# Kernel optimization log

Measured on AMD Instinct MI355X. Metric: run time of the kernel, lower is better.

The kernel has to match this reference:

```python
import jax, jax.numpy as jnp
import numpy as np

N_NODES = 50000
N_EDGES = 800000
N_GRAPHS = 128
HEADS = 4
NEG_SLOPE = 0.2


def gat_layer(x, src, dst, W, a_src, a_dst, b, n_nodes):
    # x: [N, Fin]; W: [Fin, H*Fout]; a_src/a_dst: [H, Fout]; b: [H*Fout]
    H, Fo = a_src.shape
    h = (x @ W).reshape(n_nodes, H, Fo)                      # [N, H, Fo]
    s_src = jnp.einsum('nhf,hf->nh', h, a_src)               # [N, H]
    s_dst = jnp.einsum('nhf,hf->nh', h, a_dst)               # [N, H]
    e = jax.nn.leaky_relu(s_src[src] + s_dst[dst], NEG_SLOPE)  # [E, H]
    # segment softmax over destination nodes
    emax = jax.ops.segment_max(e, dst, num_segments=n_nodes)
    ex = jnp.exp(e - emax[dst])
    denom = jax.ops.segment_sum(ex, dst, num_segments=n_nodes)
    alpha = ex / (denom[dst] + 1e-16)                        # [E, H]
    msg = h[src] * alpha[:, :, None]                         # [E, H, Fo]
    out = jax.ops.segment_sum(msg, dst, num_segments=n_nodes)
    return out.reshape(n_nodes, H * Fo) + b


def setup_inputs() -> dict:
    key = jax.random.key(0)
    ks = jax.random.split(key, 16)
    x = jax.random.normal(ks[0], (N_NODES, 128), dtype=jnp.float32)
    edge_index = jax.random.randint(ks[1], (2, N_EDGES), 0, N_NODES, dtype=jnp.int64 if jax.config.jax_enable_x64 else jnp.int32)
    batch_index = jnp.sort(jax.random.randint(ks[2], (N_NODES,), 0, N_GRAPHS))
    s = 0.1
    # layer 0: in=128 -> H=4, Fo=32  => hidden 128
    W0 = jax.random.normal(ks[3], (128, HEADS * 32), jnp.float32) * s
    a_src0 = jax.random.normal(ks[4], (HEADS, 32), jnp.float32) * s
    a_dst0 = jax.random.normal(ks[5], (HEADS, 32), jnp.float32) * s
    b0 = jnp.zeros((HEADS * 32,), jnp.float32)
    # layer 1: in=128 -> H=4, Fo=64 => hidden 256
    W1 = jax.random.normal(ks[6], (128, HEADS * 64), jnp.float32) * s
    a_src1 = jax.random.normal(ks[7], (HEADS, 64), jnp.float32) * s
    a_dst1 = jax.random.normal(ks[8], (HEADS, 64), jnp.float32) * s
    b1 = jnp.zeros((HEADS * 64,), jnp.float32)
    # layer 2: in=256 -> H=4, Fo=64 => hidden 256
    W2 = jax.random.normal(ks[9], (256, HEADS * 64), jnp.float32) * s
    a_src2 = jax.random.normal(ks[10], (HEADS, 64), jnp.float32) * s
    a_dst2 = jax.random.normal(ks[11], (HEADS, 64), jnp.float32) * s
    b2 = jnp.zeros((HEADS * 64,), jnp.float32)
    # readout linear: 512 -> 10
    Wout = jax.random.normal(ks[12], (512, 10), jnp.float32) * s
    bout = jnp.zeros((10,), jnp.float32)
    return dict(x=x, edge_index=edge_index, batch_index=batch_index,
                W0=W0, a_src0=a_src0, a_dst0=a_dst0, b0=b0,
                W1=W1, a_src1=a_src1, a_dst1=a_dst1, b1=b1,
                W2=W2, a_src2=a_src2, a_dst2=a_dst2, b2=b2,
                Wout=Wout, bout=bout)


def reference(x, edge_index, batch_index,
              W0, a_src0, a_dst0, b0,
              W1, a_src1, a_dst1, b1,
              W2, a_src2, a_dst2, b2,
              Wout, bout):
    n = x.shape[0]
    loops = jnp.arange(n, dtype=edge_index.dtype)
    src = jnp.concatenate([edge_index[0], loops])  # PyG add_self_loops
    dst = jnp.concatenate([edge_index[1], loops])
    h = jax.nn.relu(gat_layer(x, src, dst, W0, a_src0, a_dst0, b0, n))
    h = jax.nn.relu(gat_layer(h, src, dst, W1, a_src1, a_dst1, b1, n))
    h = jax.nn.relu(gat_layer(h, src, dst, W2, a_src2, a_dst2, b2, n))
    # global mean / max pool per graph
    ssum = jax.ops.segment_sum(h, batch_index, num_segments=N_GRAPHS)
    cnt = jax.ops.segment_sum(jnp.ones((n, 1), h.dtype), batch_index, num_segments=N_GRAPHS)
    gmean = ssum / jnp.maximum(cnt, 1.0)
    gmax = jax.ops.segment_max(h, batch_index, num_segments=N_GRAPHS)
    pooled = jnp.concatenate([gmean, gmax], axis=1)  # [G, 512]
    return pooled @ Wout + bout
```

## Files before the change

kernel.cpp:

```cpp
#include <hip/hip_runtime.h>
#include <cfloat>

#define N_NODES 50000
#define N_EDGES 800000
#define E_TOT   850000
#define NG      128
#define NH      4
#define CHUNK   782

typedef float f4 __attribute__((ext_vector_type(4)));
typedef float v4f __attribute__((ext_vector_type(4)));
typedef _Float16 h8v __attribute__((ext_vector_type(8)));

__global__ void count_dst_k(const int* __restrict__ ei, int* __restrict__ cnt) {
    int e = blockIdx.x * blockDim.x + threadIdx.x;
    if (e >= E_TOT) return;
    int d = (e < N_EDGES) ? ei[N_EDGES + e] : (e - N_EDGES);
    atomicAdd(&cnt[d], 1);
}

__global__ void scan_sums_k(const int* __restrict__ cnt, int* __restrict__ bsum) {
    int b = blockIdx.x;
    int start = b * CHUNK, end2 = min(start + CHUNK, N_NODES);
    int lane = threadIdx.x & 63, wv = threadIdx.x >> 6;
    int s = 0;
    for (int i = start + threadIdx.x; i < end2; i += 256) s += cnt[i];
    #pragma unroll
    for (int off = 32; off; off >>= 1) s += __shfl_xor(s, off);
    __shared__ int ws[4];
    if (lane == 0) ws[wv] = s;
    __syncthreads();
    if (threadIdx.x == 0) bsum[b] = ws[0] + ws[1] + ws[2] + ws[3];
}

__global__ void scan_off_k(int* __restrict__ bsum, int* __restrict__ row_ptr) {
    int lane = threadIdx.x;
    int v = bsum[lane];
    int s = v;
    #pragma unroll
    for (int off = 1; off < 64; off <<= 1) {
        int t = __shfl_up(s, off);
        if (lane >= off) s += t;
    }
    bsum[lane] = s - v;
    if (lane == 63) row_ptr[N_NODES] = s;
}

__global__ void scan_write_k(const int* __restrict__ cnt, const int* __restrict__ bsum,
                             int* __restrict__ row_ptr, int* __restrict__ cursor) {
    int b = blockIdx.x;
    int start = b * CHUNK, end2 = min(start + CHUNK, N_NODES);
    __shared__ int wsum[4];
    __shared__ int carry_sh;
    int lane = threadIdx.x & 63, wv = threadIdx.x >> 6;
    if (threadIdx.x == 0) carry_sh = bsum[b];
    __syncthreads();
    for (int base = start; base < end2; base += 256) {
        int i = base + threadIdx.x;
        int v = (i < end2) ? cnt[i] : 0;
        int s = v;
        #pragma unroll
        for (int off = 1; off < 64; off <<= 1) {
            int t = __shfl_up(s, off);
            if (lane >= off) s += t;
        }
        if (lane == 63) wsum[wv] = s;
        __syncthreads();
        int woff = 0;
        #pragma unroll
        for (int k = 0; k < 4; ++k) if (k < wv) woff += wsum[k];
        int carry = carry_sh;
        if (i < end2) { int rp = carry + woff + s - v; row_ptr[i] = rp; cursor[i] = rp; }
        __syncthreads();
        if (threadIdx.x == 0) carry_sh = carry + wsum[0] + wsum[1] + wsum[2] + wsum[3];
        __syncthreads();
    }
}

__global__ void fill_k(const int* __restrict__ ei, int* __restrict__ cursor,
                       int* __restrict__ col) {
    int e = blockIdx.x * blockDim.x + threadIdx.x;
    if (e >= E_TOT) return;
    int s, d;
    if (e < N_EDGES) { s = ei[e]; d = ei[N_EDGES + e]; }
    else { s = e - N_EDGES; d = s; }
    int slot = atomicAdd(&cursor[d], 1);
    __builtin_nontemporal_store(s, &col[slot]);
}

template<int K, int NOUT>
__global__ void pack_w_k(const float* __restrict__ W, _Float16* __restrict__ Wp) {
    constexpr int total = (NOUT / 16) * (K / 32) * 64;
    int t = blockIdx.x * blockDim.x + threadIdx.x;
    if (t >= total) return;
    int lane = t & 63;
    int rest = t >> 6;
    int ks = rest % (K / 32);
    int n  = rest / (K / 32);
    int colW = n * 16 + (lane & 15);
    int krow = ks * 32 + (lane >> 4) * 8;
    h8v v;
    #pragma unroll
    for (int j = 0; j < 8; ++j) v[j] = (_Float16)W[(size_t)(krow + j) * NOUT + colW];
    *(h8v*)(Wp + (size_t)t * 8) = v;
}

template<int K, int NOUT>
__global__ void pack_a_k(const float* __restrict__ W, const float* __restrict__ asrc,
                         const float* __restrict__ adst, _Float16* __restrict__ Wp) {
    constexpr int KS = K / 32;
    constexpr int NT = NOUT / 16;
    constexpr int Fo = NOUT / NH;
    int t = blockIdx.x * blockDim.x + threadIdx.x;
    if (t >= KS * 64) return;
    int ks = t >> 6, lane = t & 63;
    int colL = lane & 15;
    int krow = ks * 32 + ((lane >> 4) & 3) * 8;
    h8v v = {};
    if (colL < 8) {
        int hd = colL & 3;
        const float* av = (colL < 4) ? asrc : adst;
        #pragma unroll
        for (int j = 0; j < 8; ++j) {
            float s = 0.f;
            const float* wr = W + (size_t)(krow + j) * NOUT + hd * Fo;
            for (int f = 0; f < Fo; ++f) s += wr[f] * av[hd * Fo + f];
            v[j] = (_Float16)s;
        }
    }
    *(h8v*)(Wp + (size_t)((NT * KS + ks) * 64 + lane) * 8) = v;
}

template<int K, int NOUT, typename XT>
__global__ __launch_bounds__(256) void gemm_k(const XT* __restrict__ x,
                                              const _Float16* __restrict__ Wp,
                                              _Float16* __restrict__ outh,
                                              float* __restrict__ ssrc,
                                              float* __restrict__ sdst) {
    constexpr int SLICE = NOUT / 8;
    constexpr int KS  = K / 32;
    constexpr int NT  = NOUT / 16;
    constexpr int LK  = K + 8;
    __shared__ __align__(16) _Float16 xs[64 * LK];
    int row0 = blockIdx.x * 64;
    for (int seg = threadIdx.x; seg < 64 * K / 8; seg += 256) {
        int r = seg / (K / 8);
        int c = (seg % (K / 8)) * 8;
        h8v v = {};
        if (row0 + r < N_NODES) {
            if constexpr (sizeof(XT) == 2) {
                v = *(const h8v*)((const _Float16*)x + (size_t)(row0 + r) * K + c);
            } else {
                const float* xp = (const float*)x + (size_t)(row0 + r) * K + c;
                float4 a = *(const float4*)xp;
                float4 b = *(const float4*)(xp + 4);
                v[0] = (_Float16)a.x; v[1] = (_Float16)a.y;
                v[2] = (_Float16)a.z; v[3] = (_Float16)a.w;
                v[4] = (_Float16)b.x; v[5] = (_Float16)b.y;
                v[6] = (_Float16)b.z; v[7] = (_Float16)b.w;
            }
        }
        *(h8v*)(xs + r * LK + c) = v;
    }
    __syncthreads();
    int wv = threadIdx.x >> 6, lane = threadIdx.x & 63;
    int quad = lane >> 4, colL = lane & 15;
    int r0 = row0 + wv * 16;
    h8v afr[KS];
    #pragma unroll
    for (int ks = 0; ks < KS; ++ks)
        afr[ks] = *(const h8v*)(xs + (wv * 16 + colL) * LK + ks * 32 + quad * 8);
    const h8v* bp = (const h8v*)Wp;
    #pragma unroll
    for (int t = 0; t <= NT; ++t) {
        v4f acc = {};
        #pragma unroll
        for (int ks = 0; ks < KS; ++ks) {
            h8v bfr = bp[(size_t)(t * KS + ks) * 64 + lane];
            acc = __builtin_amdgcn_mfma_f32_16x16x32_f16(afr[ks], bfr, acc, 0, 0, 0);
        }
        if (t < NT) {
            int n0 = t * 16;
            int col = n0 + colL;
            int sl = n0 / SLICE;
            int so = col % SLICE;
            _Float16* op = outh + (size_t)sl * N_NODES * SLICE + so;
            #pragma unroll
            for (int reg = 0; reg < 4; ++reg) {
                int row = r0 + quad * 4 + reg;
                if (row < N_NODES) op[(size_t)row * SLICE] = (_Float16)acc[reg];
            }
        } else if (colL < 8) {
            int hd = colL & 3;
            float* sp = (colL < 4) ? ssrc : sdst;
            #pragma unroll
            for (int reg = 0; reg < 4; ++reg) {
                int row = r0 + quad * 4 + reg;
                if (row < N_NODES) sp[row * NH + hd] = acc[reg];
            }
        }
    }
}

__global__ __launch_bounds__(256) void alpha2_k(const float* __restrict__ ssrc,
                                                const float* __restrict__ sdst,
                                                const int* __restrict__ row_ptr,
                                                const int* __restrict__ col,
                                                float* __restrict__ alpha) {
    int wv = threadIdx.x >> 6, lane = threadIdx.x & 63;
    int grp = lane >> 4, lg = lane & 15;
    int v = blockIdx.x * 16 + wv * 4 + grp;
    if (v >= N_NODES) return;
    int beg = row_ptr[v], cnt = row_ptr[v + 1] - beg;
    f4 sdv = *(const f4*)(sdst + v * NH);
    float* pl0 = alpha + beg;
    float* pl1 = alpha + (size_t)E_TOT + beg;
    float* pl2 = alpha + (size_t)2 * E_TOT + beg;
    float* pl3 = alpha + (size_t)3 * E_TOT + beg;

    if (cnt <= 64) {
        f4 er[4];
        f4 m = {-FLT_MAX, -FLT_MAX, -FLT_MAX, -FLT_MAX};
        #pragma unroll
        for (int i = 0; i < 4; ++i) {
            int j = lg + i * 16;
            if (j < cnt) {
                int u = col[beg + j];
                f4 e = *(const f4*)(ssrc + u * NH) + sdv;
                #pragma unroll
                for (int c = 0; c < 4; ++c) e[c] = (e[c] > 0.f) ? e[c] : 0.2f * e[c];
                er[i] = e;
                #pragma unroll
                for (int c = 0; c < 4; ++c) m[c] = fmaxf(m[c], e[c]);
            }
        }
        #pragma unroll
        for (int off = 1; off < 16; off <<= 1)
            #pragma unroll
            for (int c = 0; c < 4; ++c) m[c] = fmaxf(m[c], __shfl_xor(m[c], off));
        f4 den = {};
        #pragma unroll
        for (int i = 0; i < 4; ++i) {
            int j = lg + i * 16;
            if (j < cnt) {
                f4 w;
                #pragma unroll
                for (int c = 0; c < 4; ++c) w[c] = __expf(er[i][c] - m[c]);
                er[i] = w;
                den += w;
            }
        }
        #pragma unroll
        for (int off = 1; off < 16; off <<= 1)
            #pragma unroll
            for (int c = 0; c < 4; ++c) den[c] += __shfl_xor(den[c], off);
        f4 inv;
        #pragma unroll
        for (int c = 0; c < 4; ++c) inv[c] = 1.f / (den[c] + 1e-16f);
        #pragma unroll
        for (int i = 0; i < 4; ++i) {
            int j = lg + i * 16;
            if (j < cnt) {
                pl0[j] = er[i][0] * inv[0];
                pl1[j] = er[i][1] * inv[1];
                pl2[j] = er[i][2] * inv[2];
                pl3[j] = er[i][3] * inv[3];
            }
        }
    } else {
        f4 m = {-FLT_MAX, -FLT_MAX, -FLT_MAX, -FLT_MAX};
        for (int j = lg; j < cnt; j += 16) {
            int u = col[beg + j];
            f4 e = *(const f4*)(ssrc + u * NH) + sdv;
            #pragma unroll
            for (int c = 0; c < 4; ++c) {
                e[c] = (e[c] > 0.f) ? e[c] : 0.2f * e[c];
                m[c] = fmaxf(m[c], e[c]);
            }
        }
        #pragma unroll
        for (int off = 1; off < 16; off <<= 1)
            #pragma unroll
            for (int c = 0; c < 4; ++c) m[c] = fmaxf(m[c], __shfl_xor(m[c], off));
        f4 den = {};
        for (int j = lg; j < cnt; j += 16) {
            int u = col[beg + j];
            f4 e = *(const f4*)(ssrc + u * NH) + sdv;
            #pragma unroll
            for (int c = 0; c < 4; ++c) {
                e[c] = (e[c] > 0.f) ? e[c] : 0.2f * e[c];
                den[c] += __expf(e[c] - m[c]);
            }
        }
        #pragma unroll
        for (int off = 1; off < 16; off <<= 1)
            #pragma unroll
            for (int c = 0; c < 4; ++c) den[c] += __shfl_xor(den[c], off);
        f4 inv;
        #pragma unroll
        for (int c = 0; c < 4; ++c) inv[c] = 1.f / (den[c] + 1e-16f);
        for (int j = lg; j < cnt; j += 16) {
            int u = col[beg + j];
            f4 e = *(const f4*)(ssrc + u * NH) + sdv;
            #pragma unroll
            for (int c = 0; c < 4; ++c) e[c] = (e[c] > 0.f) ? e[c] : 0.2f * e[c];
            pl0[j] = __expf(e[0] - m[0]) * inv[0];
            pl1[j] = __expf(e[1] - m[1]) * inv[1];
            pl2[j] = __expf(e[2] - m[2]) * inv[2];
            pl3[j] = __expf(e[3] - m[3]) * inv[3];
        }
    }
}

template<int HFo, int SLICE, int LPN>
__global__ __launch_bounds__(256) void agg4_k(const _Float16* __restrict__ hh,
                                              const float* __restrict__ alpha,
                                              const int* __restrict__ row_ptr,
                                              const int* __restrict__ col,
                                              const float* __restrict__ bias,
                                              _Float16* __restrict__ outH) {
    constexpr int Fo   = HFo / NH;
    constexpr int NPW  = 64 / LPN;
    constexpr int NPB  = 4 * NPW;
    constexpr int CAPW = NPW * 32;
    __shared__ int2 prS[4][CAPW];
    int s = blockIdx.x & 7;
    int g = blockIdx.x >> 3;
    int wv = threadIdx.x >> 6, lane = threadIdx.x & 63;
    int sub = lane / LPN, lq = lane % LPN;
    int vFirst = g * NPB + wv * NPW;
    if (vFirst >= N_NODES) return;
    int vCount = min(NPW, N_NODES - vFirst);
    int hd = (s * SLICE) / Fo;
    const float* ap = alpha + (size_t)hd * E_TOT;
    int begW = row_ptr[vFirst];
    int endW = row_ptr[vFirst + vCount];
    int len = endW - begW;
    bool active = sub < vCount;
    int v = vFirst + sub;
    int beg = 0, cnt = 0;
    if (active) { beg = row_ptr[v]; cnt = row_ptr[v + 1] - beg; }
    const _Float16* base = hh + (size_t)s * N_NODES * SLICE;
    unsigned fo = (unsigned)(lq * 8);
    float acc[8] = {};

    if (len <= CAPW) {
        for (int t = lane; t < len; t += 64)
            prS[wv][t] = make_int2(col[begW + t], __float_as_int(ap[begW + t]));
        __builtin_amdgcn_wave_barrier();
        int off = beg - begW;
        int j = 0;
        for (; j + 8 <= cnt; j += 8) {
            int u[8]; float w[8]; h8v hv[8];
            #pragma unroll
            for (int i = 0; i < 8; ++i) {
                int2 q = prS[wv][off + j + i];
                u[i] = q.x; w[i] = __int_as_float(q.y);
            }
            #pragma unroll
            for (int i = 0; i < 8; ++i)
                hv[i] = *(const h8v*)(base + ((unsigned)(u[i] * SLICE) + fo));
            #pragma unroll
            for (int i = 0; i < 8; ++i)
                #pragma unroll
                for (int c = 0; c < 8; ++c) acc[c] += w[i] * (float)hv[i][c];
        }
        for (; j < cnt; ++j) {
            int2 q = prS[wv][off + j];
            float w = __int_as_float(q.y);
            h8v hv = *(const h8v*)(base + ((unsigned)(q.x * SLICE) + fo));
            #pragma unroll
            for (int c = 0; c < 8; ++c) acc[c] += w * (float)hv[c];
        }
    } else {
        const int*   cp = col + beg;
        const float* app = ap + beg;
        for (int j = 0; j < cnt; ++j) {
            int u = cp[j];
            float w = app[j];
            h8v hv = *(const h8v*)(base + ((unsigned)(u * SLICE) + fo));
            #pragma unroll
            for (int c = 0; c < 8; ++c) acc[c] += w * (float)hv[c];
        }
    }
    if (active) {
        int f0 = s * SLICE + lq * 8;
        h8v res;
        #pragma unroll
        for (int c = 0; c < 8; ++c) res[c] = (_Float16)fmaxf(acc[c] + bias[f0 + c], 0.f);
        *(h8v*)(outH + (size_t)v * HFo + f0) = res;
    }
}

__global__ void pool_k(const _Float16* __restrict__ h, const int* __restrict__ batch,
                       float* __restrict__ gsum, float* __restrict__ gmax) {
    int f = threadIdx.x;
    int n0 = blockIdx.x * 32;
    int nend = min(n0 + 32, N_NODES);
    int cur = -1;
    float sa = 0.f, ma = 0.f;
    for (int n = n0; n < nend; ++n) {
        int g = batch[n];
        float val = (float)h[(size_t)n * 256 + f];
        if (g != cur) {
            if (cur >= 0) {
                atomicAdd(&gsum[cur * 256 + f], sa);
                atomicMax((int*)&gmax[cur * 256 + f], __float_as_int(ma));
            }
            cur = g; sa = 0.f; ma = 0.f;
        }
        sa += val;
        ma = fmaxf(ma, val);
    }
    if (cur >= 0) {
        atomicAdd(&gsum[cur * 256 + f], sa);
        atomicMax((int*)&gmax[cur * 256 + f], __float_as_int(ma));
    }
}

__global__ void gcnt_k(const int* __restrict__ batch, int* __restrict__ gcnt) {
    int g = threadIdx.x;
    if (g >= NG) return;
    int lo = 0, hi = N_NODES;
    while (lo < hi) { int mid = (lo + hi) >> 1; if (batch[mid] < g) lo = mid + 1; else hi = mid; }
    int b0 = lo;
    lo = 0; hi = N_NODES;
    while (lo < hi) { int mid = (lo + hi) >> 1; if (batch[mid] < g + 1) lo = mid + 1; else hi = mid; }
    gcnt[g] = lo - b0;
}

__global__ void readout_k(const float* __restrict__ gsum, const float* __restrict__ gmax,
                          const int* __restrict__ gcnt, const float* __restrict__ Wout,
                          const float* __restrict__ bout, float* __restrict__ out) {
    int g = blockIdx.x, lane = threadIdx.x;
    float inv = 1.f / fmaxf((float)gcnt[g], 1.f);
    float acc[10];
    #pragma unroll
    for (int j = 0; j < 10; ++j) acc[j] = 0.f;
    for (int f = lane; f < 512; f += 64) {
        float p = (f < 256) ? gsum[g * 256 + f] * inv : gmax[g * 256 + (f - 256)];
        #pragma unroll
        for (int j = 0; j < 10; ++j) acc[j] += p * Wout[f * 10 + j];
    }
    #pragma unroll
    for (int j = 0; j < 10; ++j) {
        float a = acc[j];
        #pragma unroll
        for (int off = 32; off; off >>= 1) a += __shfl_xor(a, off);
        if (lane == 0) out[g * 10 + j] = a + bout[j];
    }
}

extern "C" void kernel_launch(void* const* d_in, const int* in_sizes, int n_in,
                              void* d_out, int out_size, void* d_ws, size_t ws_size,
                              hipStream_t stream) {
    const float* x    = (const float*)d_in[0];
    const int*   ei   = (const int*)d_in[1];
    const int*   batch= (const int*)d_in[2];
    const float* W0   = (const float*)d_in[3];
    const float* as0  = (const float*)d_in[4];
    const float* ad0  = (const float*)d_in[5];
    const float* b0   = (const float*)d_in[6];
    const float* W1   = (const float*)d_in[7];
    const float* as1  = (const float*)d_in[8];
    const float* ad1  = (const float*)d_in[9];
    const float* b1   = (const float*)d_in[10];
    const float* W2   = (const float*)d_in[11];
    const float* as2  = (const float*)d_in[12];
    const float* ad2  = (const float*)d_in[13];
    const float* b2   = (const float*)d_in[14];
    const float* Wout = (const float*)d_in[15];
    const float* bout = (const float*)d_in[16];
    float* out = (float*)d_out;

    char* ws = (char*)d_ws;
    size_t o = 0;
    auto take = [&](size_t bytes) { size_t r = o; o += (bytes + 255) & ~(size_t)255; return r; };
    size_t cnt_o  = take((size_t)N_NODES * 4);
    size_t gsum_o = take((size_t)NG * 256 * 4);
    size_t gmax_o = take((size_t)NG * 256 * 4);
    size_t gcnt_o = take((size_t)NG * 4);
    size_t zero_bytes = o;
    size_t rp_o   = take((size_t)(N_NODES + 1) * 4);
    size_t cur_o  = take((size_t)N_NODES * 4);
    size_t bsum_o = take((size_t)64 * 4);
    size_t col_o  = take((size_t)E_TOT * 4);
    size_t ssrc_o = take((size_t)N_NODES * NH * 4);
    size_t sdst_o = take((size_t)N_NODES * NH * 4);
    size_t alp_o  = take((size_t)NH * E_TOT * 4);
    size_t hh_o   = take((size_t)N_NODES * 256 * 2);
    size_t bufH_o = take((size_t)N_NODES * 256 * 2);
    size_t wp0_o  = take((size_t)(8 + 1) * 4 * 64 * 8 * 2);
    size_t wp1_o  = take((size_t)(16 + 1) * 4 * 64 * 8 * 2);
    size_t wp2_o  = take((size_t)(16 + 1) * 8 * 64 * 8 * 2);

    int*      cnt    = (int*)(ws + cnt_o);
    float*    gsum   = (float*)(ws + gsum_o);
    float*    gmax   = (float*)(ws + gmax_o);
    int*      gcnt   = (int*)(ws + gcnt_o);
    int*      row_ptr= (int*)(ws + rp_o);
    int*      cursor = (int*)(ws + cur_o);
    int*      bsum   = (int*)(ws + bsum_o);
    int*      col    = (int*)(ws + col_o);
    float*    ssrc   = (float*)(ws + ssrc_o);
    float*    sdst   = (float*)(ws + sdst_o);
    float*    alpha  = (float*)(ws + alp_o);
    _Float16* hH     = (_Float16*)(ws + hh_o);
    _Float16* bufH   = (_Float16*)(ws + bufH_o);
    _Float16* Wp0    = (_Float16*)(ws + wp0_o);
    _Float16* Wp1    = (_Float16*)(ws + wp1_o);
    _Float16* Wp2    = (_Float16*)(ws + wp2_o);

    (void)hipMemsetAsync(ws, 0, zero_bytes, stream);

    count_dst_k<<<(E_TOT + 255) / 256, 256, 0, stream>>>(ei, cnt);
    scan_sums_k<<<64, 256, 0, stream>>>(cnt, bsum);
    scan_off_k<<<1, 64, 0, stream>>>(bsum, row_ptr);
    scan_write_k<<<64, 256, 0, stream>>>(cnt, bsum, row_ptr, cursor);
    fill_k<<<(E_TOT + 255) / 256, 256, 0, stream>>>(ei, cursor, col);

    pack_w_k<128, 128><<<8, 256, 0, stream>>>(W0, Wp0);
    pack_w_k<128, 256><<<16, 256, 0, stream>>>(W1, Wp1);
    pack_w_k<256, 256><<<32, 256, 0, stream>>>(W2, Wp2);
    pack_a_k<128, 128><<<1, 256, 0, stream>>>(W0, as0, ad0, Wp0);
    pack_a_k<128, 256><<<1, 256, 0, stream>>>(W1, as1, ad1, Wp1);
    pack_a_k<256, 256><<<2, 256, 0, stream>>>(W2, as2, ad2, Wp2);

    int gemm_grid  = (N_NODES + 63) / 64;
    int alpha_grid = (N_NODES + 15) / 16;
    int agg128_grid = 8 * ((N_NODES + 127) / 128);
    int agg256_grid = 8 * ((N_NODES + 63) / 64);

    gemm_k<128, 128, float><<<gemm_grid, 256, 0, stream>>>(x, Wp0, hH, ssrc, sdst);
    alpha2_k<<<alpha_grid, 256, 0, stream>>>(ssrc, sdst, row_ptr, col, alpha);
    agg4_k<128, 16, 2><<<agg128_grid, 256, 0, stream>>>(hH, alpha, row_ptr, col, b0, bufH);

    gemm_k<128, 256, _Float16><<<gemm_grid, 256, 0, stream>>>(bufH, Wp1, hH, ssrc, sdst);
    alpha2_k<<<alpha_grid, 256, 0, stream>>>(ssrc, sdst, row_ptr, col, alpha);
    agg4_k<256, 32, 4><<<agg256_grid, 256, 0, stream>>>(hH, alpha, row_ptr, col, b1, bufH);

    gemm_k<256, 256, _Float16><<<gemm_grid, 256, 0, stream>>>(bufH, Wp2, hH, ssrc, sdst);
    alpha2_k<<<alpha_grid, 256, 0, stream>>>(ssrc, sdst, row_ptr, col, alpha);
    agg4_k<256, 32, 4><<<agg256_grid, 256, 0, stream>>>(hH, alpha, row_ptr, col, b2, bufH);

    pool_k<<<(N_NODES + 31) / 32, 256, 0, stream>>>(bufH, batch, gsum, gmax);
    gcnt_k<<<1, 128, 0, stream>>>(batch, gcnt);
    readout_k<<<NG, 64, 0, stream>>>(gsum, gmax, gcnt, Wout, bout, out);
}
```

Measured before the change: 517.2 us.

## Merge pack and count launches, add direct-load fp16 GEMM, vectorize pooling

Merges the six weight-packing launches into two kernels and folds the per-graph node count into the readout kernel, which cuts the number of small launches. Adds a GEMM variant for the fp16 hidden layers that loads A fragments straight from global memory with no LDS staging and computes 128 rows per block, reusing each B fragment for two row tiles. Pooling now handles two features per thread with half2 loads and runs with 128 threads per block. The col store in fill_k drops its nontemporal hint. The costs are more registers in the new GEMM and uncoalesced global fragment loads in place of LDS reads.

Result: faster. 476.9 us (-7.8%).

```diff
diff --git a/kernel.cpp b/kernel.cpp
--- a/kernel.cpp
+++ b/kernel.cpp
@@ -10,6 +10,7 @@
 
 typedef float f4 __attribute__((ext_vector_type(4)));
 typedef float v4f __attribute__((ext_vector_type(4)));
+typedef _Float16 h2v __attribute__((ext_vector_type(2)));
 typedef _Float16 h8v __attribute__((ext_vector_type(8)));
 
 __global__ void count_dst_k(const int* __restrict__ ei, int* __restrict__ cnt) {
@@ -85,14 +86,13 @@
     if (e < N_EDGES) { s = ei[e]; d = ei[N_EDGES + e]; }
     else { s = e - N_EDGES; d = s; }
     int slot = atomicAdd(&cursor[d], 1);
-    __builtin_nontemporal_store(s, &col[slot]);
+    col[slot] = s;
 }
 
 template<int K, int NOUT>
-__global__ void pack_w_k(const float* __restrict__ W, _Float16* __restrict__ Wp) {
-    constexpr int total = (NOUT / 16) * (K / 32) * 64;
-    int t = blockIdx.x * blockDim.x + threadIdx.x;
-    if (t >= total) return;
+__device__ void pack_w_dev(const float* __restrict__ W, _Float16* __restrict__ Wp, int blk) {
+    int t = blk * 256 + threadIdx.x;
+    if (t >= (NOUT / 16) * (K / 32) * 64) return;
     int lane = t & 63;
     int rest = t >> 6;
     int ks = rest % (K / 32);
@@ -105,13 +105,22 @@
     *(h8v*)(Wp + (size_t)t * 8) = v;
 }
 
+__global__ void pack_w_all_k(const float* __restrict__ W0, const float* __restrict__ W1,
+                             const float* __restrict__ W2, _Float16* __restrict__ Wp0,
+                             _Float16* __restrict__ Wp1, _Float16* __restrict__ Wp2) {
+    int b = blockIdx.x;
+    if (b < 8)       pack_w_dev<128, 128>(W0, Wp0, b);
+    else if (b < 24) pack_w_dev<128, 256>(W1, Wp1, b - 8);
+    else             pack_w_dev<256, 256>(W2, Wp2, b - 24);
+}
+
 template<int K, int NOUT>
-__global__ void pack_a_k(const float* __restrict__ W, const float* __restrict__ asrc,
-                         const float* __restrict__ adst, _Float16* __restrict__ Wp) {
+__device__ void pack_a_dev(const float* __restrict__ W, const float* __restrict__ asrc,
+                           const float* __restrict__ adst, _Float16* __restrict__ Wp, int blk) {
     constexpr int KS = K / 32;
     constexpr int NT = NOUT / 16;
     constexpr int Fo = NOUT / NH;
-    int t = blockIdx.x * blockDim.x + threadIdx.x;
+    int t = blk * 256 + threadIdx.x;
     if (t >= KS * 64) return;
     int ks = t >> 6, lane = t & 63;
     int colL = lane & 15;
@@ -131,8 +140,20 @@
     *(h8v*)(Wp + (size_t)((NT * KS + ks) * 64 + lane) * 8) = v;
 }
 
-template<int K, int NOUT, typename XT>
-__global__ __launch_bounds__(256) void gemm_k(const XT* __restrict__ x,
+__global__ void pack_a_all_k(const float* __restrict__ W0, const float* __restrict__ as0,
+                             const float* __restrict__ ad0, _Float16* __restrict__ Wp0,
+                             const float* __restrict__ W1, const float* __restrict__ as1,
+                             const float* __restrict__ ad1, _Float16* __restrict__ Wp1,
+                             const float* __restrict__ W2, const float* __restrict__ as2,
+                             const float* __restrict__ ad2, _Float16* __restrict__ Wp2) {
+    int b = blockIdx.x;
+    if (b == 0)      pack_a_dev<128, 128>(W0, as0, ad0, Wp0, 0);
+    else if (b == 1) pack_a_dev<128, 256>(W1, as1, ad1, Wp1, 0);
+    else             pack_a_dev<256, 256>(W2, as2, ad2, Wp2, b - 2);
+}
+
+template<int K, int NOUT>
+__global__ __launch_bounds__(256) void gemm_k(const float* __restrict__ x,
                                               const _Float16* __restrict__ Wp,
                                               _Float16* __restrict__ outh,
                                               float* __restrict__ ssrc,
@@ -148,17 +169,13 @@
         int c = (seg % (K / 8)) * 8;
         h8v v = {};
         if (row0 + r < N_NODES) {
-            if constexpr (sizeof(XT) == 2) {
-                v = *(const h8v*)((const _Float16*)x + (size_t)(row0 + r) * K + c);
-            } else {
-                const float* xp = (const float*)x + (size_t)(row0 + r) * K + c;
-                float4 a = *(const float4*)xp;
-                float4 b = *(const float4*)(xp + 4);
-                v[0] = (_Float16)a.x; v[1] = (_Float16)a.y;
-                v[2] = (_Float16)a.z; v[3] = (_Float16)a.w;
-                v[4] = (_Float16)b.x; v[5] = (_Float16)b.y;
-                v[6] = (_Float16)b.z; v[7] = (_Float16)b.w;
-            }
+            const float* xp = x + (size_t)(row0 + r) * K + c;
+            float4 a = *(const float4*)xp;
+            float4 b = *(const float4*)(xp + 4);
+            v[0] = (_Float16)a.x; v[1] = (_Float16)a.y;
+            v[2] = (_Float16)a.z; v[3] = (_Float16)a.w;
+            v[4] = (_Float16)b.x; v[5] = (_Float16)b.y;
+            v[6] = (_Float16)b.z; v[7] = (_Float16)b.w;
         }
         *(h8v*)(xs + r * LK + c) = v;
     }
@@ -197,6 +214,65 @@
             for (int reg = 0; reg < 4; ++reg) {
                 int row = r0 + quad * 4 + reg;
                 if (row < N_NODES) sp[row * NH + hd] = acc[reg];
+            }
+        }
+    }
+}
+
+template<int K, int NOUT>
+__global__ __launch_bounds__(256) void gemm_h_k(const _Float16* __restrict__ x,
+                                                const _Float16* __restrict__ Wp,
+                                                _Float16* __restrict__ outh,
+                                                float* __restrict__ ssrc,
+                                                float* __restrict__ sdst) {
+    constexpr int SLICE = NOUT / 8;
+    constexpr int KS = K / 32;
+    constexpr int NT = NOUT / 16;
+    int wv = threadIdx.x >> 6, lane = threadIdx.x & 63;
+    int quad = lane >> 4, colL = lane & 15;
+    int row0 = blockIdx.x * 128;
+    int r0a = row0 + wv * 16;
+    int r0b = row0 + 64 + wv * 16;
+    int rA = min(r0a + colL, N_NODES - 1);
+    int rB = min(r0b + colL, N_NODES - 1);
+    h8v afrA[KS], afrB[KS];
+    #pragma unroll
+    for (int ks = 0; ks < KS; ++ks) {
+        afrA[ks] = *(const h8v*)(x + (size_t)rA * K + ks * 32 + quad * 8);
+        afrB[ks] = *(const h8v*)(x + (size_t)rB * K + ks * 32 + quad * 8);
+    }
+    const h8v* bp = (const h8v*)Wp;
+    #pragma unroll
+    for (int t = 0; t <= NT; ++t) {
+        v4f accA = {}, accB = {};
+        #pragma unroll
+        for (int ks = 0; ks < KS; ++ks) {
+            h8v bfr = bp[(size_t)(t * KS + ks) * 64 + lane];
+            accA = __builtin_amdgcn_mfma_f32_16x16x32_f16(afrA[ks], bfr, accA, 0, 0, 0);
+            accB = __builtin_amdgcn_mfma_f32_16x16x32_f16(afrB[ks], bfr, accB, 0, 0, 0);
+        }
+        if (t < NT) {
+            int n0 = t * 16;
+            int col = n0 + colL;
+            int sl = n0 / SLICE;
+            int so = col % SLICE;
+            _Float16* op = outh + (size_t)sl * N_NODES * SLICE + so;
+            #pragma unroll
+            for (int reg = 0; reg < 4; ++reg) {
+                int rowA = r0a + quad * 4 + reg;
+                int rowB = r0b + quad * 4 + reg;
+                if (rowA < N_NODES) op[(size_t)rowA * SLICE] = (_Float16)accA[reg];
+                if (rowB < N_NODES) op[(size_t)rowB * SLICE] = (_Float16)accB[reg];
+            }
+        } else if (colL < 8) {
+            int hd = colL & 3;
+            float* sp = (colL < 4) ? ssrc : sdst;
+            #pragma unroll
+            for (int reg = 0; reg < 4; ++reg) {
+                int rowA = r0a + quad * 4 + reg;
+                int rowB = r0b + quad * 4 + reg;
+                if (rowA < N_NODES) sp[rowA * NH + hd] = accA[reg];
+                if (rowB < N_NODES) sp[rowB * NH + hd] = accB[reg];
             }
         }
     }
@@ -394,46 +470,45 @@
 
 __global__ void pool_k(const _Float16* __restrict__ h, const int* __restrict__ batch,
                        float* __restrict__ gsum, float* __restrict__ gmax) {
-    int f = threadIdx.x;
+    int f2 = threadIdx.x * 2;
     int n0 = blockIdx.x * 32;
     int nend = min(n0 + 32, N_NODES);
     int cur = -1;
-    float sa = 0.f, ma = 0.f;
+    float sa0 = 0.f, sa1 = 0.f, ma0 = 0.f, ma1 = 0.f;
     for (int n = n0; n < nend; ++n) {
         int g = batch[n];
-        float val = (float)h[(size_t)n * 256 + f];
+        h2v val = *(const h2v*)(h + (size_t)n * 256 + f2);
+        float v0 = (float)val[0], v1 = (float)val[1];
         if (g != cur) {
             if (cur >= 0) {
-                atomicAdd(&gsum[cur * 256 + f], sa);
-                atomicMax((int*)&gmax[cur * 256 + f], __float_as_int(ma));
-            }
-            cur = g; sa = 0.f; ma = 0.f;
-        }
-        sa += val;
-        ma = fmaxf(ma, val);
+                atomicAdd(&gsum[cur * 256 + f2], sa0);
+                atomicAdd(&gsum[cur * 256 + f2 + 1], sa1);
+                atomicMax((int*)&gmax[cur * 256 + f2], __float_as_int(ma0));
+                atomicMax((int*)&gmax[cur * 256 + f2 + 1], __float_as_int(ma1));
+            }
+            cur = g; sa0 = sa1 = 0.f; ma0 = ma1 = 0.f;
+        }
+        sa0 += v0; sa1 += v1;
+        ma0 = fmaxf(ma0, v0); ma1 = fmaxf(ma1, v1);
     }
     if (cur >= 0) {
-        atomicAdd(&gsum[cur * 256 + f], sa);
-        atomicMax((int*)&gmax[cur * 256 + f], __float_as_int(ma));
-    }
-}
-
-__global__ void gcnt_k(const int* __restrict__ batch, int* __restrict__ gcnt) {
-    int g = threadIdx.x;
-    if (g >= NG) return;
+        atomicAdd(&gsum[cur * 256 + f2], sa0);
+        atomicAdd(&gsum[cur * 256 + f2 + 1], sa1);
+        atomicMax((int*)&gmax[cur * 256 + f2], __float_as_int(ma0));
+        atomicMax((int*)&gmax[cur * 256 + f2 + 1], __float_as_int(ma1));
+    }
+}
+
+__global__ void readout_k(const float* __restrict__ gsum, const float* __restrict__ gmax,
+                          const int* __restrict__ batch, const float* __restrict__ Wout,
+                          const float* __restrict__ bout, float* __restrict__ out) {
+    int g = blockIdx.x, lane = threadIdx.x;
     int lo = 0, hi = N_NODES;
     while (lo < hi) { int mid = (lo + hi) >> 1; if (batch[mid] < g) lo = mid + 1; else hi = mid; }
     int b0 = lo;
     lo = 0; hi = N_NODES;
     while (lo < hi) { int mid = (lo + hi) >> 1; if (batch[mid] < g + 1) lo = mid + 1; else hi = mid; }
-    gcnt[g] = lo - b0;
-}
-
-__global__ void readout_k(const float* __restrict__ gsum, const float* __restrict__ gmax,
-                          const int* __restrict__ gcnt, const float* __restrict__ Wout,
-                          const float* __restrict__ bout, float* __restrict__ out) {
-    int g = blockIdx.x, lane = threadIdx.x;
-    float inv = 1.f / fmaxf((float)gcnt[g], 1.f);
+    float inv = 1.f / fmaxf((float)(lo - b0), 1.f);
     float acc[10];
     #pragma unroll
     for (int j = 0; j < 10; ++j) acc[j] = 0.f;
@@ -479,7 +554,6 @@
     size_t cnt_o  = take((size_t)N_NODES * 4);
     size_t gsum_o = take((size_t)NG * 256 * 4);
     size_t gmax_o = take((size_t)NG * 256 * 4);
-    size_t gcnt_o = take((size_t)NG * 4);
     size_t zero_bytes = o;
     size_t rp_o   = take((size_t)(N_NODES + 1) * 4);
     size_t cur_o  = take((size_t)N_NODES * 4);
@@ -497,7 +571,6 @@
     int*      cnt    = (int*)(ws + cnt_o);
     float*    gsum   = (float*)(ws + gsum_o);
     float*    gmax   = (float*)(ws + gmax_o);
-    int*      gcnt   = (int*)(ws + gcnt_o);
     int*      row_ptr= (int*)(ws + rp_o);
     int*      cursor = (int*)(ws + cur_o);
     int*      bsum   = (int*)(ws + bsum_o);
@@ -519,31 +592,28 @@
     scan_write_k<<<64, 256, 0, stream>>>(cnt, bsum, row_ptr, cursor);
     fill_k<<<(E_TOT + 255) / 256, 256, 0, stream>>>(ei, cursor, col);
 
-    pack_w_k<128, 128><<<8, 256, 0, stream>>>(W0, Wp0);
-    pack_w_k<128, 256><<<16, 256, 0, stream>>>(W1, Wp1);
-    pack_w_k<256, 256><<<32, 256, 0, stream>>>(W2, Wp2);
-    pack_a_k<128, 128><<<1, 256, 0, stream>>>(W0, as0, ad0, Wp0);
-    pack_a_k<128, 256><<<1, 256, 0, stream>>>(W1, as1, ad1, Wp1);
-    pack_a_k<256, 256><<<2, 256, 0, stream>>>(W2, as2, ad2, Wp2);
-
-    int gemm_grid  = (N_NODES + 63) / 64;
+    pack_w_all_k<<<56, 256, 0, stream>>>(W0, W1, W2, Wp0, Wp1, Wp2);
+    pack_a_all_k<<<4, 256, 0, stream>>>(W0, as0, ad0, Wp0, W1, as1, ad1, Wp1,
+                                        W2, as2, ad2, Wp2);
+
+    int gemm0_grid = (N_NODES + 63) / 64;
+    int gemmh_grid = (N_NODES + 127) / 128;
     int alpha_grid = (N_NODES + 15) / 16;
     int agg128_grid = 8 * ((N_NODES + 127) / 128);
     int agg256_grid = 8 * ((N_NODES + 63) / 64);
 
-    gemm_k<128, 128, float><<<gemm_grid, 256, 0, stream>>>(x, Wp0, hH, ssrc, sdst);
+    gemm_k<128, 128><<<gemm0_grid, 256, 0, stream>>>(x, Wp0, hH, ssrc, sdst);
     alpha2_k<<<alpha_grid, 256, 0, stream>>>(ssrc, sdst, row_ptr, col, alpha);
     agg4_k<128, 16, 2><<<agg128_grid, 256, 0, stream>>>(hH, alpha, row_ptr, col, b0, bufH);
 
-    gemm_k<128, 256, _Float16><<<gemm_grid, 256, 0, stream>>>(bufH, Wp1, hH, ssrc, sdst);
+    gemm_h_k<128, 256><<<gemmh_grid, 256, 0, stream>>>(bufH, Wp1, hH, ssrc, sdst);
     alpha2_k<<<alpha_grid, 256, 0, stream>>>(ssrc, sdst, row_ptr, col, alpha);
     agg4_k<256, 32, 4><<<agg256_grid, 256, 0, stream>>>(hH, alpha, row_ptr, col, b1, bufH);
 
-    gemm_k<256, 256, _Float16><<<gemm_grid, 256, 0, stream>>>(bufH, Wp2, hH, ssrc, sdst);
+    gemm_h_k<256, 256><<<gemmh_grid, 256, 0, stream>>>(bufH, Wp2, hH, ssrc, sdst);
     alpha2_k<<<alpha_grid, 256, 0, stream>>>(ssrc, sdst, row_ptr, col, alpha);
     agg4_k<256, 32, 4><<<agg256_grid, 256, 0, stream>>>(hH, alpha, row_ptr, col, b2, bufH);
 
-    pool_k<<<(N_NODES + 31) / 32, 256, 0, stream>>>(bufH, batch, gsum, gmax);
-    gcnt_k<<<1, 128, 0, stream>>>(batch, gcnt);
-    readout_k<<<NG, 64, 0, stream>>>(gsum, gmax, gcnt, Wout, bout, out);
-}
+    pool_k<<<(N_NODES + 31) / 32, 128, 0, stream>>>(bufH, batch, gsum, gmax);
+    readout_k<<<NG, 64, 0, stream>>>(gsum, gmax, batch, Wout, bout, out);
+}
```
